# Kernel tuning notes

Hardware: AMD Instinct MI355X
Metric: run time of the kernel (lower is better)

Reference implementation:

```python
import jax, jax.numpy as jnp
import numpy as np


def conv2d(x, w, b, pad):
    y = jax.lax.conv_general_dilated(x, w, (1, 1), [(pad, pad), (pad, pad)],
                                     dimension_numbers=('NCHW', 'OIHW', 'NCHW'))
    return y + b[None, :, None, None]


def setup_inputs() -> dict:
    key = jax.random.key(0)
    ks = jax.random.split(key, 24)
    bs, C, OC, K = 2, 64, 3, 3
    hi = wi = 96
    ho = wo = 192

    def _w(k, o, i, kh, kw):
        return jax.random.normal(k, (o, i, kh, kw), jnp.float32) / np.float32(np.sqrt(i * kh * kw))

    inp = {
        'x': jax.random.normal(ks[0], (bs, C, hi, wi), jnp.float32),
        'poseMap': jax.random.normal(ks[1], (1, 3, ho, wo), jnp.float32),
        'interMapY': jax.random.randint(ks[2], (ho, wo), 0, hi, jnp.int32),
        'interMapX': jax.random.randint(ks[3], (ho, wo), 0, wi, jnp.int32),
        # sigmaconv: 3x3 convs 64->64->64->2
        'sig_w1': _w(ks[4], 64, 64, 3, 3), 'sig_b1': jnp.zeros((64,), jnp.float32),
        'sig_w2': _w(ks[5], 64, 64, 3, 3), 'sig_b2': jnp.zeros((64,), jnp.float32),
        'sig_w3': _w(ks[6], 2, 64, 3, 3), 'sig_b3': jnp.zeros((2,), jnp.float32),
        # dwconv: 1x1 convs 3->64->256->C*K*K
        'dw_w1': _w(ks[7], 64, 3, 1, 1), 'dw_b1': jnp.zeros((64,), jnp.float32),
        'dw_w2': _w(ks[8], 256, 64, 1, 1), 'dw_b2': jnp.zeros((256,), jnp.float32),
        'dw_w3': _w(ks[9], C * K * K, 256, 1, 1), 'dw_b3': jnp.zeros((C * K * K,), jnp.float32),
        # pwconv: 1x1 convs 3->64->256->C*OC
        'pw_w1': _w(ks[10], 64, 3, 1, 1), 'pw_b1': jnp.zeros((64,), jnp.float32),
        'pw_w2': _w(ks[11], 256, 64, 1, 1), 'pw_b2': jnp.zeros((256,), jnp.float32),
        'pw_w3': _w(ks[12], C * OC, 256, 1, 1), 'pw_b3': jnp.zeros((C * OC,), jnp.float32),
    }
    return inp


def reference(x, poseMap, interMapY, interMapX,
              sig_w1, sig_b1, sig_w2, sig_b2, sig_w3, sig_b3,
              dw_w1, dw_b1, dw_w2, dw_b2, dw_w3, dw_b3,
              pw_w1, pw_b1, pw_w2, pw_b2, pw_w3, pw_b3):
    C, K, OC = 64, 3, 3
    bs, _, hi, wi = x.shape
    ho, wo = poseMap.shape[2], poseMap.shape[3]
    pad = K // 2

    p = jax.lax.stop_gradient(poseMap)  # original detaches poseMap
    # kernel-predict branches (1x1 conv MLPs over position map)
    dw = conv2d(jax.nn.relu(conv2d(jax.nn.relu(conv2d(p, dw_w1, dw_b1, 0)), dw_w2, dw_b2, 0)), dw_w3, dw_b3, 0)
    dw = dw.reshape(1, C, K * K, ho, wo)
    pw = conv2d(jax.nn.relu(conv2d(jax.nn.relu(conv2d(p, pw_w1, pw_b1, 0)), pw_w2, pw_b2, 0)), pw_w3, pw_b3, 0)
    pw = pw.reshape(C, OC, ho, wo)

    # unfold(x, K, padding=K//2): [bs, C, K*K, hi, wi], kernel taps row-major
    xp = jnp.pad(x, ((0, 0), (0, 0), (pad, pad), (pad, pad)))
    h = jnp.stack([xp[:, :, dy:dy + hi, dx:dx + wi]
                   for dy in range(K) for dx in range(K)], axis=2)
    # irregular spatial gather to HR grid: [bs, C, K*K, ho, wo]
    h = h[:, :, :, interMapY, interMapX]

    mean = jnp.sum(h * jax.nn.softmax(dw, axis=2), axis=2)  # [bs, C, ho, wo]
    sigma = conv2d(jax.nn.relu(conv2d(jax.nn.relu(conv2d(mean, sig_w1, sig_b1, 1)), sig_w2, sig_b2, 1)), sig_w3, sig_b3, 1)
    sigmad = sigma[:, 0:1, None, :, :]
    sigmar = sigma[:, 1:2, None, :, :]
    bw = sigmad * dw + sigmar * jnp.abs(h - mean[:, :, None, :, :])
    xa = jnp.sum(h * jax.nn.softmax(bw, axis=2), axis=2)  # [bs, C, ho, wo]
    out = jnp.einsum('bchw,cohw->bohw', xa, pw)  # [bs, OC, ho, wo]
    return out
```

## Files before the change

kernel.cpp:

```cpp
#include <hip/hip_runtime.h>

#define NPIX 36864

typedef __attribute__((ext_vector_type(8))) short short8;
typedef __attribute__((ext_vector_type(4))) short short4v;
typedef __attribute__((ext_vector_type(4))) float float4v;

__device__ inline unsigned short f2b(float x) {
    unsigned int u = __float_as_uint(x);
    unsigned int r = (u + 0x7FFFu + ((u >> 16) & 1u)) >> 16;
    return (unsigned short)r;
}
__device__ inline float b2f(unsigned short h) {
    return __uint_as_float(((unsigned int)h) << 16);
}

#define WB_TOTAL 312320
#define XCAST_N  1179648
__global__ __launch_bounds__(256) void prep_all(
    const float* __restrict__ dw2, const float* __restrict__ dw3,
    const float* __restrict__ pw2, const float* __restrict__ pw3,
    const float* __restrict__ sw1, const float* __restrict__ sw2,
    const float* __restrict__ sw3, unsigned short* __restrict__ wb,
    const float* __restrict__ x, unsigned short* __restrict__ xb)
{
    int i = blockIdx.x * 256 + threadIdx.x;
    if (i >= WB_TOTAL) {
        int j = i - WB_TOTAL;
        if (j < XCAST_N) xb[j] = f2b(x[j]);
        return;
    }
    unsigned short v;
    if (i < 16384)        v = f2b(dw2[i]);
    else if (i < 32768)   v = f2b(pw2[i - 16384]);
    else if (i < 180224)  v = f2b(dw3[i - 32768]);
    else if (i < 229376)  v = f2b(pw3[i - 180224]);
    else if (i < 266240) { int j = i - 229376; int t = j / 4096, r = j % 4096, oc = r / 64, ic = r % 64;
                           v = f2b(sw1[(oc * 64 + ic) * 9 + t]); }
    else if (i < 303104) { int j = i - 266240; int t = j / 4096, r = j % 4096, oc = r / 64, ic = r % 64;
                           v = f2b(sw2[(oc * 64 + ic) * 9 + t]); }
    else                 { int j = i - 303104; int t = j / 1024, r = j % 1024, oc = r / 64, ic = r % 64;
                           v = (oc < 2) ? f2b(sw3[(oc * 64 + ic) * 9 + t]) : (unsigned short)0; }
    wb[i] = v;
}

__global__ __launch_bounds__(256) void l1_k(
    const float* __restrict__ pose,
    const float* __restrict__ wA, const float* __restrict__ bA,
    const float* __restrict__ wB, const float* __restrict__ bB,
    unsigned short* __restrict__ out)
{
    int px = blockIdx.x * 256 + threadIdx.x;
    int chain = blockIdx.y;
    const float* w = chain ? wB : wA;
    const float* bi = chain ? bB : bA;
    float p0 = pose[px], p1 = pose[NPIX + px], p2 = pose[2 * NPIX + px];
    unsigned int pk[32];
    #pragma unroll
    for (int c = 0; c < 64; ++c) {
        float v = bi[c] + w[c * 3] * p0 + w[c * 3 + 1] * p1 + w[c * 3 + 2] * p2;
        v = fmaxf(v, 0.f);
        unsigned short u = f2b(v);
        if (c & 1) pk[c >> 1] |= ((unsigned int)u) << 16; else pk[c >> 1] = u;
    }
    uint4* o = (uint4*)&out[((size_t)chain * NPIX + px) * 64];
    #pragma unroll
    for (int q = 0; q < 8; ++q) o[q] = ((uint4*)pk)[q];
}

template<int K>
__global__ __launch_bounds__(256) void gemm_dual(
    const unsigned short* __restrict__ actA, const unsigned short* __restrict__ actB,
    const unsigned short* __restrict__ wgtA, const unsigned short* __restrict__ wgtB,
    const float* __restrict__ biasA, const float* __restrict__ biasB,
    unsigned short* __restrict__ outA, unsigned short* __restrict__ outB,
    int tilesA, int octotA, int octotB, int relu)
{
    constexpr int KP = K + 8;
    __shared__ unsigned short Bs[256 * KP];
    unsigned short* Ts = Bs;
    const int tid = threadIdx.x;
    const int px0 = blockIdx.x * 256;
    const bool second = (int)blockIdx.y >= tilesA;
    const int oc0 = (second ? blockIdx.y - tilesA : blockIdx.y) * 64;
    const unsigned short* act = second ? actB : actA;
    const unsigned short* wgt = second ? wgtB : wgtA;
    const float* bias = second ? biasB : biasA;
    unsigned short* outp = second ? outB : outA;
    const int octot = second ? octotB : octotA;
    const int w = tid >> 6, l = tid & 63;
    const int ln = l & 15, lkg = l >> 4, lk = lkg * 8;
    const int ocA = oc0 + w * 16 + ln;
    short8 Ar[2];
    Ar[0] = *(const short8*)&wgt[(size_t)ocA * K + lk];
    Ar[1] = *(const short8*)&wgt[(size_t)ocA * K + 32 + lk];
    for (int idx = tid; idx < 256 * (K / 8); idx += 256) {
        int p = idx >> 3, ko = (idx & 7) * 8;
        *(short8*)&Bs[p * KP + ko] = *(const short8*)&act[(size_t)(px0 + p) * K + ko];
    }
    __syncthreads();
    float4v acc[16] = {};
    #pragma unroll
    for (int kc = 0; kc < 2; ++kc) {
        #pragma unroll
        for (int nt = 0; nt < 16; ++nt) {
            short8 b = *(const short8*)&Bs[(nt * 16 + ln) * KP + kc * 32 + lk];
            acc[nt] = __builtin_amdgcn_mfma_f32_16x16x32_bf16(Ar[kc], b, acc[nt], 0, 0, 0);
        }
    }
    __syncthreads();
    float bv[4];
    #pragma unroll
    for (int r = 0; r < 4; ++r) bv[r] = bias[oc0 + w * 16 + lkg * 4 + r];
    #pragma unroll
    for (int nt = 0; nt < 16; ++nt) {
        int pxl = nt * 16 + ln;
        #pragma unroll
        for (int r = 0; r < 4; ++r) {
            float v = acc[nt][r] + bv[r];
            if (relu) v = fmaxf(v, 0.f);
            Ts[pxl * KP + w * 16 + lkg * 4 + r] = f2b(v);
        }
    }
    __syncthreads();
    for (int c = tid; c < 2048; c += 256) {
        int pxl = c >> 3, ch = (c & 7) * 8;
        *(short8*)&outp[(size_t)(px0 + pxl) * octot + oc0 + ch] = *(const short8*)&Ts[pxl * KP + ch];
    }
}

__global__ __launch_bounds__(256) void gemm_l3(
    const unsigned short* __restrict__ actA, const unsigned short* __restrict__ actB,
    const unsigned short* __restrict__ wgt,
    const float* __restrict__ biasA, const float* __restrict__ biasB,
    unsigned short* __restrict__ outA, unsigned short* __restrict__ outB)
{
    __shared__ unsigned short Bs[128 * 264];
    unsigned short* Ts = Bs;
    const int tid = threadIdx.x;
    const int px0 = blockIdx.x * 128;
    const int mb  = blockIdx.y;
    const unsigned short* act = (mb < 3) ? actA : actB;
    const int w = tid >> 6, l = tid & 63;
    const int ln = l & 15, lkg = l >> 4, lk = lkg * 8;
    const int row0 = mb * 192 + w * 48 + ln;
    for (int idx = tid; idx < 128 * 32; idx += 256) {
        int p = idx >> 5, ko = (idx & 31) * 8;
        *(short8*)&Bs[p * 264 + ko] = *(const short8*)&act[(size_t)(px0 + p) * 256 + ko];
    }
    __syncthreads();
    float4v acc[3][8] = {};
    #pragma unroll
    for (int kc = 0; kc < 8; ++kc) {
        short8 a0 = *(const short8*)&wgt[(size_t)(row0 +  0) * 256 + kc * 32 + lk];
        short8 a1 = *(const short8*)&wgt[(size_t)(row0 + 16) * 256 + kc * 32 + lk];
        short8 a2 = *(const short8*)&wgt[(size_t)(row0 + 32) * 256 + kc * 32 + lk];
        #pragma unroll
        for (int nt = 0; nt < 8; ++nt) {
            short8 b = *(const short8*)&Bs[(nt * 16 + ln) * 264 + kc * 32 + lk];
            acc[0][nt] = __builtin_amdgcn_mfma_f32_16x16x32_bf16(a0, b, acc[0][nt], 0, 0, 0);
            acc[1][nt] = __builtin_amdgcn_mfma_f32_16x16x32_bf16(a1, b, acc[1][nt], 0, 0, 0);
            acc[2][nt] = __builtin_amdgcn_mfma_f32_16x16x32_bf16(a2, b, acc[2][nt], 0, 0, 0);
        }
    }
    __syncthreads();
    #pragma unroll
    for (int mt = 0; mt < 3; ++mt) {
        int rowb = w * 48 + mt * 16 + lkg * 4;
        #pragma unroll
        for (int r = 0; r < 4; ++r) {
            int goc = mb * 192 + rowb + r;
            float bv = (goc < 576) ? biasA[goc] : biasB[goc - 576];
            #pragma unroll
            for (int nt = 0; nt < 8; ++nt)
                Ts[(rowb + r) * 136 + nt * 16 + ln] = f2b(acc[mt][nt][r] + bv);
        }
    }
    __syncthreads();
    for (int c = tid; c < 3072; c += 256) {
        int row = c >> 4, ch = (c & 15) * 8;
        int goc = mb * 192 + row;
        unsigned short* dst = (goc < 576) ? (outA + (size_t)goc * NPIX)
                                          : (outB + (size_t)(goc - 576) * NPIX);
        *(short8*)&dst[px0 + ch] = *(const short8*)&Ts[row * 136 + ch];
    }
}

template<int MT>
__global__ __launch_bounds__(256) void conv3x3_mfma(
    const unsigned short* __restrict__ act, const unsigned short* __restrict__ wgt,
    const float* __restrict__ bias, unsigned short* __restrict__ out,
    int relu)
{
    constexpr int SP = 72;
    constexpr int OCP = MT * 16;
    __shared__ unsigned short Bs[3 * 66 * SP];
    const int tid = threadIdx.x;
    int bx = blockIdx.x;
    const int xt = bx % 3; bx /= 3;
    const int y = bx % 192; const int b = bx / 192;
    const int x0 = xt * 64;
    const size_t actb = (size_t)b * NPIX * 64;
    const int w = tid >> 6, l = tid & 63;
    const int ln = l & 15, lkg = l >> 4, lk = lkg * 8;
    const int mt = (MT == 4) ? w : 0;
    short8 Wr[9][2];
    #pragma unroll
    for (int t = 0; t < 9; ++t)
        #pragma unroll
        for (int hh = 0; hh < 2; ++hh)
            Wr[t][hh] = *(const short8*)&wgt[((size_t)t * OCP + mt * 16 + ln) * 64 + hh * 32 + lk];
    for (int s = tid; s < 198; s += 256) {
        int r = s / 66, i = s % 66;
        int yy = y + r - 1, xx = x0 + i - 1;
        unsigned short* dst = &Bs[(r * 66 + i) * SP];
        if (yy >= 0 && yy < 192 && xx >= 0 && xx < 192) {
            const unsigned short* src = &act[actb + (size_t)(yy * 192 + xx) * 64];
            #pragma unroll
            for (int j = 0; j < 8; ++j) *(short8*)(dst + j * 8) = *(const short8*)(src + j * 8);
        } else {
            short8 z = {};
            #pragma unroll
            for (int j = 0; j < 8; ++j) *(short8*)(dst + j * 8) = z;
        }
    }
    __syncthreads();
    const int NT = (MT == 4) ? 4 : 1;
    const int ntb = (MT == 4) ? 0 : w;
    float4v acc[4] = {{0,0,0,0},{0,0,0,0},{0,0,0,0},{0,0,0,0}};
    #pragma unroll
    for (int t = 0; t < 9; ++t) {
        const int r = t / 3, dx = t % 3;
        #pragma unroll
        for (int hh = 0; hh < 2; ++hh) {
            #pragma unroll
            for (int n = 0; n < 4; ++n) {
                if (n >= NT) break;
                int slot = r * 66 + (ntb + n) * 16 + ln + dx;
                short8 bf = *(const short8*)&Bs[slot * SP + hh * 32 + lk];
                acc[n] = __builtin_amdgcn_mfma_f32_16x16x32_bf16(Wr[t][hh], bf, acc[n], 0, 0, 0);
            }
        }
    }
    #pragma unroll
    for (int n = 0; n < 4; ++n) {
        if (n >= NT) break;
        int px = y * 192 + x0 + (ntb + n) * 16 + ln;
        if (MT == 4) {
            int oc = mt * 16 + lkg * 4;
            float v0 = acc[n][0] + bias[oc + 0];
            float v1 = acc[n][1] + bias[oc + 1];
            float v2 = acc[n][2] + bias[oc + 2];
            float v3 = acc[n][3] + bias[oc + 3];
            if (relu) { v0 = fmaxf(v0, 0.f); v1 = fmaxf(v1, 0.f); v2 = fmaxf(v2, 0.f); v3 = fmaxf(v3, 0.f); }
            uint2 pk;
            pk.x = (unsigned int)f2b(v0) | (((unsigned int)f2b(v1)) << 16);
            pk.y = (unsigned int)f2b(v2) | (((unsigned int)f2b(v3)) << 16);
            *(uint2*)&out[((size_t)b * NPIX + px) * 64 + oc] = pk;
        } else if (lkg == 0) {
            float v0 = acc[n][0] + bias[0];
            float v1 = acc[n][1] + bias[1];
            out[((size_t)b * 2 + 0) * NPIX + px] = f2b(v0);
            out[((size_t)b * 2 + 1) * NPIX + px] = f2b(v1);
        }
    }
}

#define PLSZ 10192
__device__ inline void stage_planes(const unsigned short* __restrict__ xb, int c,
                                    unsigned short* __restrict__ pl, int tid)
{
    short8 z = {};
    short8* pf = (short8*)pl;
    for (int i = tid; i < (2 * PLSZ) / 8; i += 256) pf[i] = z;
    __syncthreads();
    #pragma unroll
    for (int b = 0; b < 2; ++b) {
        const unsigned short* xp = xb + (size_t)(b * 64 + c) * 9216;
        unsigned short* pb = pl + b * PLSZ;
        for (int i = tid; i < 96 * 12; i += 256) {
            int row = i / 12, ch = i % 12;
            const short4v* src = (const short4v*)&xp[row * 96 + ch * 8];
            unsigned short* d = &pb[(row + 1) * 104 + 4 + ch * 8];
            *(short4v*)d = src[0];
            *(short4v*)(d + 4) = src[1];
        }
    }
    __syncthreads();
}

__global__ __launch_bounds__(256) void mean_k(
    const unsigned short* __restrict__ xb, const int* __restrict__ imy, const int* __restrict__ imx,
    const unsigned short* __restrict__ dw, unsigned short* __restrict__ mean_cm)
{
    __shared__ unsigned short pl[2 * PLSZ];
    const int c = blockIdx.y;
    const int px0 = blockIdx.x * 1024;
    const int tid = threadIdx.x;
    stage_planes(xb, c, pl, tid);
    #pragma unroll
    for (int q = 0; q < 4; ++q) {
        int px = px0 + q * 256 + tid;
        int base = imy[px] * 104 + imx[px] + 3;
        float wk[9];
        {
            float d[9];
            #pragma unroll
            for (int k = 0; k < 9; ++k) d[k] = b2f(dw[(size_t)(c * 9 + k) * NPIX + px]);
            float m = d[0];
            #pragma unroll
            for (int k = 1; k < 9; ++k) m = fmaxf(m, d[k]);
            float s = 0.f;
            #pragma unroll
            for (int k = 0; k < 9; ++k) { wk[k] = __expf(d[k] - m); s += wk[k]; }
            float inv = 1.f / s;
            #pragma unroll
            for (int k = 0; k < 9; ++k) wk[k] *= inv;
        }
        #pragma unroll
        for (int b = 0; b < 2; ++b) {
            const unsigned short* pb = pl + b * PLSZ;
            float a = 0.f;
            #pragma unroll
            for (int k = 0; k < 9; ++k)
                a += wk[k] * b2f(pb[base + (k / 3) * 104 + (k % 3)]);
            mean_cm[(size_t)(b * 64 + c) * NPIX + px] = f2b(a);
        }
    }
}

__global__ __launch_bounds__(256) void tr_k(
    const unsigned short* __restrict__ in, unsigned short* __restrict__ out)
{
    __shared__ unsigned short T[64 * 68];
    int px0 = blockIdx.x * 64;
    int b = blockIdx.y;
    int tid = threadIdx.x;
    for (int i = tid; i < 4096; i += 256) {
        int c = i >> 6, p = i & 63;
        T[p * 68 + c] = in[(size_t)(b * 64 + c) * NPIX + px0 + p];
    }
    __syncthreads();
    for (int i = tid; i < 4096; i += 256) {
        int p = i >> 6, c = i & 63;
        out[((size_t)b * NPIX + px0 + p) * 64 + c] = T[p * 68 + c];
    }
}

__global__ __launch_bounds__(256) void xa_k(
    const unsigned short* __restrict__ xb, const int* __restrict__ imy, const int* __restrict__ imx,
    const unsigned short* __restrict__ dw, const unsigned short* __restrict__ mean_cm,
    const unsigned short* __restrict__ sigma, unsigned short* __restrict__ xab)
{
    __shared__ unsigned short pl[2 * PLSZ];
    const int c = blockIdx.y;
    const int px0 = blockIdx.x * 1024;
    const int tid = threadIdx.x;
    stage_planes(xb, c, pl, tid);
    #pragma unroll
    for (int q = 0; q < 4; ++q) {
        int px = px0 + q * 256 + tid;
        int base = imy[px] * 104 + imx[px] + 3;
        float d[9];
        #pragma unroll
        for (int k = 0; k < 9; ++k) d[k] = b2f(dw[(size_t)(c * 9 + k) * NPIX + px]);
        #pragma unroll
        for (int b = 0; b < 2; ++b) {
            const unsigned short* pb = pl + b * PLSZ;
            float mn = b2f(mean_cm[(size_t)(b * 64 + c) * NPIX + px]);
            float sd = b2f(sigma[((size_t)b * 2 + 0) * NPIX + px]);
            float sr = b2f(sigma[((size_t)b * 2 + 1) * NPIX + px]);
            float h[9], bw[9];
            #pragma unroll
            for (int k = 0; k < 9; ++k) {
                h[k] = b2f(pb[base + (k / 3) * 104 + (k % 3)]);
                bw[k] = sd * d[k] + sr * fabsf(h[k] - mn);
            }
            float m = bw[0];
            #pragma unroll
            for (int k = 1; k < 9; ++k) m = fmaxf(m, bw[k]);
            float s = 0.f, a = 0.f;
            #pragma unroll
            for (int k = 0; k < 9; ++k) { float e = __expf(bw[k] - m); s += e; a += e * h[k]; }
            xab[(size_t)(b * 64 + c) * NPIX + px] = f2b(a / s);
        }
    }
}

__global__ __launch_bounds__(256) void einsum_part(
    const unsigned short* __restrict__ xab, const unsigned short* __restrict__ pw,
    float* __restrict__ part)
{
    int px = blockIdx.x * 256 + threadIdx.x;
    int b = blockIdx.y;
    int c0 = blockIdx.z * 16;
    float a0 = 0.f, a1 = 0.f, a2 = 0.f;
    #pragma unroll
    for (int c = 0; c < 16; ++c) {
        float v = b2f(xab[(size_t)(b * 64 + c0 + c) * NPIX + px]);
        a0 += v * b2f(pw[(size_t)((c0 + c) * 3 + 0) * NPIX + px]);
        a1 += v * b2f(pw[(size_t)((c0 + c) * 3 + 1) * NPIX + px]);
        a2 += v * b2f(pw[(size_t)((c0 + c) * 3 + 2) * NPIX + px]);
    }
    size_t base = ((size_t)blockIdx.z * 6 + b * 3) * NPIX + px;
    part[base + 0 * NPIX] = a0;
    part[base + 1 * NPIX] = a1;
    part[base + 2 * NPIX] = a2;
}

__global__ __launch_bounds__(256) void einsum_red(
    const float* __restrict__ part, float* __restrict__ out)
{
    int i = blockIdx.x * 256 + threadIdx.x;
    float s = part[i] + part[(size_t)6 * NPIX + i] + part[(size_t)12 * NPIX + i] + part[(size_t)18 * NPIX + i];
    out[i] = s;
}

extern "C" void kernel_launch(void* const* d_in, const int* in_sizes, int n_in,
                              void* d_out, int out_size, void* d_ws, size_t ws_size,
                              hipStream_t stream)
{
    (void)in_sizes; (void)n_in; (void)out_size; (void)ws_size;
    const float* x      = (const float*)d_in[0];
    const float* pose   = (const float*)d_in[1];
    const int*   imy    = (const int*)d_in[2];
    const int*   imx    = (const int*)d_in[3];
    const float* sig_w1 = (const float*)d_in[4];
    const float* sig_b1 = (const float*)d_in[5];
    const float* sig_w2 = (const float*)d_in[6];
    const float* sig_b2 = (const float*)d_in[7];
    const float* sig_w3 = (const float*)d_in[8];
    const float* sig_b3 = (const float*)d_in[9];
    const float* dw_w1  = (const float*)d_in[10];
    const float* dw_b1  = (const float*)d_in[11];
    const float* dw_w2  = (const float*)d_in[12];
    const float* dw_b2  = (const float*)d_in[13];
    const float* dw_w3  = (const float*)d_in[14];
    const float* dw_b3  = (const float*)d_in[15];
    const float* pw_w1  = (const float*)d_in[16];
    const float* pw_b1  = (const float*)d_in[17];
    const float* pw_w2  = (const float*)d_in[18];
    const float* pw_b2  = (const float*)d_in[19];
    const float* pw_w3  = (const float*)d_in[20];
    const float* pw_b3  = (const float*)d_in[21];
    float* out = (float*)d_out;

    unsigned short* ws = (unsigned short*)d_ws;
    size_t off = 0;
    unsigned short* wb      = ws + off; off += WB_TOTAL;
    unsigned short* xb16    = ws + off; off += (size_t)XCAST_N;
    unsigned short* h1      = ws + off; off += (size_t)2 * NPIX * 64;
    unsigned short* h2      = ws + off; off += (size_t)2 * NPIX * 256;
    unsigned short* dwbuf   = ws + off; off += (size_t)576 * NPIX;
    unsigned short* pwbuf   = ws + off; off += (size_t)192 * NPIX;
    unsigned short* mean_cm = ws + off; off += (size_t)2 * 64 * NPIX;
    unsigned short* mean_pm = ws + off; off += (size_t)2 * NPIX * 64;
    unsigned short* s1      = ws + off; off += (size_t)2 * NPIX * 64;
    unsigned short* s2      = ws + off; off += (size_t)2 * NPIX * 64;
    unsigned short* sigma   = ws + off; off += (size_t)2 * 2 * NPIX;
    unsigned short* xab     = ws + off; off += (size_t)2 * 64 * NPIX;
    off = (off + 1) & ~(size_t)1;
    float* part = (float*)(ws + off);

    unsigned short* w_dw2 = wb + 0;
    unsigned short* w_pw2 = wb + 16384;
    unsigned short* w_33  = wb + 32768;
    unsigned short* w_s1t = wb + 229376;
    unsigned short* w_s2t = wb + 266240;
    unsigned short* w_s3t = wb + 303104;

    unsigned short* h1dw = h1;
    unsigned short* h1pw = h1 + (size_t)NPIX * 64;
    unsigned short* h2dw = h2;
    unsigned short* h2pw = h2 + (size_t)NPIX * 256;

    dim3 blk(256);
    prep_all<<<dim3((WB_TOTAL + XCAST_N + 255) / 256), blk, 0, stream>>>(
        dw_w2, dw_w3, pw_w2, pw_w3, sig_w1, sig_w2, sig_w3, wb, x, xb16);
    l1_k<<<dim3(144, 2), blk, 0, stream>>>(pose, dw_w1, dw_b1, pw_w1, pw_b1, h1);
    gemm_dual<64><<<dim3(144, 8), blk, 0, stream>>>(
        h1dw, h1pw, w_dw2, w_pw2, dw_b2, pw_b2, h2dw, h2pw, 4, 256, 256, 1);
    gemm_l3<<<dim3(288, 4), blk, 0, stream>>>(
        h2dw, h2pw, w_33, dw_b3, pw_b3, dwbuf, pwbuf);
    mean_k<<<dim3(36, 64), blk, 0, stream>>>(xb16, imy, imx, dwbuf, mean_cm);
    tr_k<<<dim3(576, 2), blk, 0, stream>>>(mean_cm, mean_pm);
    conv3x3_mfma<4><<<dim3(1152), blk, 0, stream>>>(mean_pm, w_s1t, sig_b1, s1, 1);
    conv3x3_mfma<4><<<dim3(1152), blk, 0, stream>>>(s1,      w_s2t, sig_b2, s2, 1);
    conv3x3_mfma<1><<<dim3(1152), blk, 0, stream>>>(s2,      w_s3t, sig_b3, sigma, 0);
    xa_k<<<dim3(36, 64), blk, 0, stream>>>(xb16, imy, imx, dwbuf, mean_cm, sigma, xab);
    einsum_part<<<dim3(144, 2, 4), blk, 0, stream>>>(xab, pwbuf, part);
    einsum_red<<<dim3(864), blk, 0, stream>>>(part, out);
}
```

Before: 277.2 us.

## Fuse three-layer kernel-predict MLPs into one kernel keeping hidden layers in LDS

Replaces the separate layer-1, layer-2 and layer-3 kernels of the dw/pw position MLPs with a single kernel that processes 64-pixel tiles per chain. Hidden activations h1 and h2 now stay in shared memory instead of round-tripping through global memory, which removes two launches and the associated HBM traffic. In exchange the dw chain block loops over three output chunks while the pw chain does only one, so the two kinds of block do unequal work. The smaller pixel tile also means layer-2 and layer-3 weights are re-read from global or cache more often per pixel.

```diff
diff --git a/kernel.cpp b/kernel.cpp
--- a/kernel.cpp
+++ b/kernel.cpp
@@ -44,145 +44,107 @@
     wb[i] = v;
 }
 
-__global__ __launch_bounds__(256) void l1_k(
+__global__ __launch_bounds__(256) void mlp_fused(
     const float* __restrict__ pose,
-    const float* __restrict__ wA, const float* __restrict__ bA,
-    const float* __restrict__ wB, const float* __restrict__ bB,
-    unsigned short* __restrict__ out)
-{
-    int px = blockIdx.x * 256 + threadIdx.x;
-    int chain = blockIdx.y;
-    const float* w = chain ? wB : wA;
-    const float* bi = chain ? bB : bA;
-    float p0 = pose[px], p1 = pose[NPIX + px], p2 = pose[2 * NPIX + px];
-    unsigned int pk[32];
-    #pragma unroll
-    for (int c = 0; c < 64; ++c) {
-        float v = bi[c] + w[c * 3] * p0 + w[c * 3 + 1] * p1 + w[c * 3 + 2] * p2;
-        v = fmaxf(v, 0.f);
-        unsigned short u = f2b(v);
-        if (c & 1) pk[c >> 1] |= ((unsigned int)u) << 16; else pk[c >> 1] = u;
-    }
-    uint4* o = (uint4*)&out[((size_t)chain * NPIX + px) * 64];
-    #pragma unroll
-    for (int q = 0; q < 8; ++q) o[q] = ((uint4*)pk)[q];
-}
-
-template<int K>
-__global__ __launch_bounds__(256) void gemm_dual(
-    const unsigned short* __restrict__ actA, const unsigned short* __restrict__ actB,
-    const unsigned short* __restrict__ wgtA, const unsigned short* __restrict__ wgtB,
-    const float* __restrict__ biasA, const float* __restrict__ biasB,
-    unsigned short* __restrict__ outA, unsigned short* __restrict__ outB,
-    int tilesA, int octotA, int octotB, int relu)
-{
-    constexpr int KP = K + 8;
-    __shared__ unsigned short Bs[256 * KP];
-    unsigned short* Ts = Bs;
+    const float* __restrict__ w1A, const float* __restrict__ b1A,
+    const float* __restrict__ w1B, const float* __restrict__ b1B,
+    const unsigned short* __restrict__ w2A, const unsigned short* __restrict__ w2B,
+    const float* __restrict__ b2A, const float* __restrict__ b2B,
+    const unsigned short* __restrict__ w33,
+    const float* __restrict__ b3A, const float* __restrict__ b3B,
+    unsigned short* __restrict__ outA, unsigned short* __restrict__ outB)
+{
+    __shared__ unsigned short h1s[64 * 72];
+    __shared__ unsigned short h2s[64 * 264];
+    __shared__ unsigned short Ts[192 * 72];
     const int tid = threadIdx.x;
-    const int px0 = blockIdx.x * 256;
-    const bool second = (int)blockIdx.y >= tilesA;
-    const int oc0 = (second ? blockIdx.y - tilesA : blockIdx.y) * 64;
-    const unsigned short* act = second ? actB : actA;
-    const unsigned short* wgt = second ? wgtB : wgtA;
-    const float* bias = second ? biasB : biasA;
-    unsigned short* outp = second ? outB : outA;
-    const int octot = second ? octotB : octotA;
+    const int chain = blockIdx.y;
+    const int px0 = blockIdx.x * 64;
     const int w = tid >> 6, l = tid & 63;
     const int ln = l & 15, lkg = l >> 4, lk = lkg * 8;
-    const int ocA = oc0 + w * 16 + ln;
-    short8 Ar[2];
-    Ar[0] = *(const short8*)&wgt[(size_t)ocA * K + lk];
-    Ar[1] = *(const short8*)&wgt[(size_t)ocA * K + 32 + lk];
-    for (int idx = tid; idx < 256 * (K / 8); idx += 256) {
-        int p = idx >> 3, ko = (idx & 7) * 8;
-        *(short8*)&Bs[p * KP + ko] = *(const short8*)&act[(size_t)(px0 + p) * K + ko];
-    }
-    __syncthreads();
-    float4v acc[16] = {};
-    #pragma unroll
-    for (int kc = 0; kc < 2; ++kc) {
-        #pragma unroll
-        for (int nt = 0; nt < 16; ++nt) {
-            short8 b = *(const short8*)&Bs[(nt * 16 + ln) * KP + kc * 32 + lk];
-            acc[nt] = __builtin_amdgcn_mfma_f32_16x16x32_bf16(Ar[kc], b, acc[nt], 0, 0, 0);
-        }
-    }
-    __syncthreads();
-    float bv[4];
-    #pragma unroll
-    for (int r = 0; r < 4; ++r) bv[r] = bias[oc0 + w * 16 + lkg * 4 + r];
-    #pragma unroll
-    for (int nt = 0; nt < 16; ++nt) {
-        int pxl = nt * 16 + ln;
-        #pragma unroll
-        for (int r = 0; r < 4; ++r) {
-            float v = acc[nt][r] + bv[r];
-            if (relu) v = fmaxf(v, 0.f);
-            Ts[pxl * KP + w * 16 + lkg * 4 + r] = f2b(v);
-        }
-    }
-    __syncthreads();
-    for (int c = tid; c < 2048; c += 256) {
-        int pxl = c >> 3, ch = (c & 7) * 8;
-        *(short8*)&outp[(size_t)(px0 + pxl) * octot + oc0 + ch] = *(const short8*)&Ts[pxl * KP + ch];
-    }
-}
-
-__global__ __launch_bounds__(256) void gemm_l3(
-    const unsigned short* __restrict__ actA, const unsigned short* __restrict__ actB,
-    const unsigned short* __restrict__ wgt,
-    const float* __restrict__ biasA, const float* __restrict__ biasB,
-    unsigned short* __restrict__ outA, unsigned short* __restrict__ outB)
-{
-    __shared__ unsigned short Bs[128 * 264];
-    unsigned short* Ts = Bs;
-    const int tid = threadIdx.x;
-    const int px0 = blockIdx.x * 128;
-    const int mb  = blockIdx.y;
-    const unsigned short* act = (mb < 3) ? actA : actB;
-    const int w = tid >> 6, l = tid & 63;
-    const int ln = l & 15, lkg = l >> 4, lk = lkg * 8;
-    const int row0 = mb * 192 + w * 48 + ln;
-    for (int idx = tid; idx < 128 * 32; idx += 256) {
-        int p = idx >> 5, ko = (idx & 31) * 8;
-        *(short8*)&Bs[p * 264 + ko] = *(const short8*)&act[(size_t)(px0 + p) * 256 + ko];
-    }
-    __syncthreads();
-    float4v acc[3][8] = {};
-    #pragma unroll
-    for (int kc = 0; kc < 8; ++kc) {
-        short8 a0 = *(const short8*)&wgt[(size_t)(row0 +  0) * 256 + kc * 32 + lk];
-        short8 a1 = *(const short8*)&wgt[(size_t)(row0 + 16) * 256 + kc * 32 + lk];
-        short8 a2 = *(const short8*)&wgt[(size_t)(row0 + 32) * 256 + kc * 32 + lk];
-        #pragma unroll
-        for (int nt = 0; nt < 8; ++nt) {
-            short8 b = *(const short8*)&Bs[(nt * 16 + ln) * 264 + kc * 32 + lk];
-            acc[0][nt] = __builtin_amdgcn_mfma_f32_16x16x32_bf16(a0, b, acc[0][nt], 0, 0, 0);
-            acc[1][nt] = __builtin_amdgcn_mfma_f32_16x16x32_bf16(a1, b, acc[1][nt], 0, 0, 0);
-            acc[2][nt] = __builtin_amdgcn_mfma_f32_16x16x32_bf16(a2, b, acc[2][nt], 0, 0, 0);
-        }
-    }
-    __syncthreads();
-    #pragma unroll
-    for (int mt = 0; mt < 3; ++mt) {
-        int rowb = w * 48 + mt * 16 + lkg * 4;
-        #pragma unroll
-        for (int r = 0; r < 4; ++r) {
-            int goc = mb * 192 + rowb + r;
-            float bv = (goc < 576) ? biasA[goc] : biasB[goc - 576];
-            #pragma unroll
-            for (int nt = 0; nt < 8; ++nt)
-                Ts[(rowb + r) * 136 + nt * 16 + ln] = f2b(acc[mt][nt][r] + bv);
-        }
-    }
-    __syncthreads();
-    for (int c = tid; c < 3072; c += 256) {
-        int row = c >> 4, ch = (c & 15) * 8;
-        int goc = mb * 192 + row;
-        unsigned short* dst = (goc < 576) ? (outA + (size_t)goc * NPIX)
-                                          : (outB + (size_t)(goc - 576) * NPIX);
-        *(short8*)&dst[px0 + ch] = *(const short8*)&Ts[row * 136 + ch];
+    const float* w1 = chain ? w1B : w1A;
+    const float* b1 = chain ? b1B : b1A;
+    const unsigned short* w2 = chain ? w2B : w2A;
+    const float* b2 = chain ? b2B : b2A;
+    {
+        int px = px0 + l;
+        float p0 = pose[px], p1 = pose[NPIX + px], p2 = pose[2 * NPIX + px];
+        #pragma unroll
+        for (int j = 0; j < 16; ++j) {
+            int oc = w * 16 + j;
+            float v = b1[oc] + w1[oc * 3] * p0 + w1[oc * 3 + 1] * p1 + w1[oc * 3 + 2] * p2;
+            h1s[l * 72 + oc] = f2b(fmaxf(v, 0.f));
+        }
+    }
+    __syncthreads();
+    {
+        float4v acc[4][4] = {};
+        #pragma unroll
+        for (int mt = 0; mt < 4; ++mt) {
+            int ocr = w * 64 + mt * 16 + ln;
+            short8 a0 = *(const short8*)&w2[(size_t)ocr * 64 + lk];
+            short8 a1 = *(const short8*)&w2[(size_t)ocr * 64 + 32 + lk];
+            #pragma unroll
+            for (int nt = 0; nt < 4; ++nt) {
+                short8 b0 = *(const short8*)&h1s[(nt * 16 + ln) * 72 + lk];
+                short8 b1v = *(const short8*)&h1s[(nt * 16 + ln) * 72 + 32 + lk];
+                acc[mt][nt] = __builtin_amdgcn_mfma_f32_16x16x32_bf16(a0, b0, acc[mt][nt], 0, 0, 0);
+                acc[mt][nt] = __builtin_amdgcn_mfma_f32_16x16x32_bf16(a1, b1v, acc[mt][nt], 0, 0, 0);
+            }
+        }
+        #pragma unroll
+        for (int mt = 0; mt < 4; ++mt) {
+            int ocb = w * 64 + mt * 16 + lkg * 4;
+            float bv0 = b2[ocb + 0], bv1 = b2[ocb + 1], bv2 = b2[ocb + 2], bv3 = b2[ocb + 3];
+            #pragma unroll
+            for (int nt = 0; nt < 4; ++nt) {
+                int pxl = nt * 16 + ln;
+                h2s[pxl * 264 + ocb + 0] = f2b(fmaxf(acc[mt][nt][0] + bv0, 0.f));
+                h2s[pxl * 264 + ocb + 1] = f2b(fmaxf(acc[mt][nt][1] + bv1, 0.f));
+                h2s[pxl * 264 + ocb + 2] = f2b(fmaxf(acc[mt][nt][2] + bv2, 0.f));
+                h2s[pxl * 264 + ocb + 3] = f2b(fmaxf(acc[mt][nt][3] + bv3, 0.f));
+            }
+        }
+    }
+    __syncthreads();
+    const int nchunk = chain ? 1 : 3;
+    const float* b3 = chain ? b3B : b3A;
+    unsigned short* outp = chain ? outB : outA;
+    for (int ch = 0; ch < nchunk; ++ch) {
+        const int rowbase = chain ? 576 : ch * 192;
+        const int obase   = ch * 192;
+        float4v acc[3][4] = {};
+        const int r0 = rowbase + w * 48 + ln;
+        #pragma unroll
+        for (int kc = 0; kc < 8; ++kc) {
+            short8 a0 = *(const short8*)&w33[(size_t)(r0 +  0) * 256 + kc * 32 + lk];
+            short8 a1 = *(const short8*)&w33[(size_t)(r0 + 16) * 256 + kc * 32 + lk];
+            short8 a2 = *(const short8*)&w33[(size_t)(r0 + 32) * 256 + kc * 32 + lk];
+            #pragma unroll
+            for (int nt = 0; nt < 4; ++nt) {
+                short8 b = *(const short8*)&h2s[(nt * 16 + ln) * 264 + kc * 32 + lk];
+                acc[0][nt] = __builtin_amdgcn_mfma_f32_16x16x32_bf16(a0, b, acc[0][nt], 0, 0, 0);
+                acc[1][nt] = __builtin_amdgcn_mfma_f32_16x16x32_bf16(a1, b, acc[1][nt], 0, 0, 0);
+                acc[2][nt] = __builtin_amdgcn_mfma_f32_16x16x32_bf16(a2, b, acc[2][nt], 0, 0, 0);
+            }
+        }
+        #pragma unroll
+        for (int mt = 0; mt < 3; ++mt) {
+            int rowb = w * 48 + mt * 16 + lkg * 4;
+            #pragma unroll
+            for (int r = 0; r < 4; ++r) {
+                float bv = b3[obase + rowb + r];
+                #pragma unroll
+                for (int nt = 0; nt < 4; ++nt)
+                    Ts[(rowb + r) * 72 + nt * 16 + ln] = f2b(acc[mt][nt][r] + bv);
+            }
+        }
+        __syncthreads();
+        for (int i = tid; i < 1536; i += 256) {
+            int row = i >> 3, pc = (i & 7) * 8;
+            *(short8*)&outp[(size_t)(obase + row) * NPIX + px0 + pc] = *(const short8*)&Ts[row * 72 + pc];
+        }
+        __syncthreads();
     }
 }
 
@@ -449,8 +411,6 @@
     size_t off = 0;
     unsigned short* wb      = ws + off; off += WB_TOTAL;
     unsigned short* xb16    = ws + off; off += (size_t)XCAST_N;
-    unsigned short* h1      = ws + off; off += (size_t)2 * NPIX * 64;
-    unsigned short* h2      = ws + off; off += (size_t)2 * NPIX * 256;
     unsigned short* dwbuf   = ws + off; off += (size_t)576 * NPIX;
     unsigned short* pwbuf   = ws + off; off += (size_t)192 * NPIX;
     unsigned short* mean_cm = ws + off; off += (size_t)2 * 64 * NPIX;
@@ -469,19 +429,12 @@
     unsigned short* w_s2t = wb + 266240;
     unsigned short* w_s3t = wb + 303104;
 
-    unsigned short* h1dw = h1;
-    unsigned short* h1pw = h1 + (size_t)NPIX * 64;
-    unsigned short* h2dw = h2;
-    unsigned short* h2pw = h2 + (size_t)NPIX * 256;
-
     dim3 blk(256);
     prep_all<<<dim3((WB_TOTAL + XCAST_N + 255) / 256), blk, 0, stream>>>(
         dw_w2, dw_w3, pw_w2, pw_w3, sig_w1, sig_w2, sig_w3, wb, x, xb16);
-    l1_k<<<dim3(144, 2), blk, 0, stream>>>(pose, dw_w1, dw_b1, pw_w1, pw_b1, h1);
-    gemm_dual<64><<<dim3(144, 8), blk, 0, stream>>>(
-        h1dw, h1pw, w_dw2, w_pw2, dw_b2, pw_b2, h2dw, h2pw, 4, 256, 256, 1);
-    gemm_l3<<<dim3(288, 4), blk, 0, stream>>>(
-        h2dw, h2pw, w_33, dw_b3, pw_b3, dwbuf, pwbuf);
+    mlp_fused<<<dim3(576, 2), blk, 0, stream>>>(
+        pose, dw_w1, dw_b1, pw_w1, pw_b1, w_dw2, w_pw2, dw_b2, pw_b2,
+        w_33, dw_b3, pw_b3, dwbuf, pwbuf);
     mean_k<<<dim3(36, 64), blk, 0, stream>>>(xb16, imy, imx, dwbuf, mean_cm);
     tr_k<<<dim3(576, 2), blk, 0, stream>>>(mean_cm, mean_pm);
     conv3x3_mfma<4><<<dim3(1152), blk, 0, stream>>>(mean_pm, w_s1t, sig_b1, s1, 1);
```

New measurement: 266.8 us. 3.8% less time.
